# Optimization experiments

Measured on AMD Instinct MI355X. Metric: run time of the kernel, lower is better.

The kernel has to match this reference:

```python
import jax, jax.numpy as jnp
import numpy as np

TAU = 0.01
RHO = 1.99
SIGMA = 1.0 / TAU / 72.0  # 1/tau/72 as in __init__
N_IT = 10  # n_it_max


def nabla2(x):
    # forward finite differences: channel 0 along W (last axis), channel 1 along H
    u = jnp.zeros(x.shape + (2,), x.dtype)
    u = u.at[..., :, :-1, 0].add(x[..., :, 1:] - x[..., :, :-1])
    u = u.at[..., :-1, :, 1].add(x[..., 1:, :] - x[..., :-1, :])
    return u


def nabla2_adjoint(u):
    x = jnp.zeros(u.shape[:-1], u.dtype)
    x = x.at[..., :, :-1].add(-u[..., :, :-1, 0])
    x = x.at[..., :, 1:].add(u[..., :, :-1, 0])
    x = x.at[..., :-1, :].add(-u[..., :-1, :, 1])
    x = x.at[..., 1:, :].add(u[..., :-1, :, 1])
    return x


def epsilon2(I):
    # Jacobian of the vector field I [..., H, W, 2] -> G [..., H, W, 4]
    I0, I1 = I[..., 0], I[..., 1]
    G = jnp.zeros(I0.shape + (4,), I.dtype)
    G = G.at[..., 0].add(I0)                                  # G0 = I0 - shift_H(I0)
    G = G.at[..., 1:, :, 0].add(-I0[..., :-1, :])
    G = G.at[..., :, 1:, 1].add(I0[..., :, 1:] - I0[..., :, :-1])  # G1: W-diff of I0
    G = G.at[..., 2].add(I1)                                  # G2 = I1 - shift_W(I1)
    G = G.at[..., :, 1:, 2].add(-I1[..., :, :-1])
    G = G.at[..., :-1, :, 3].add(I1[..., 1:, :] - I1[..., :-1, :])  # G3: H-diff of I1
    return G


def epsilon2_adjoint(G):
    I = jnp.zeros(G.shape[:-1] + (2,), G.dtype)
    I = I.at[..., 0].add(G[..., 0])
    I = I.at[..., :-1, :, 0].add(-G[..., 1:, :, 0])
    I = I.at[..., :, :-1, 0].add(-G[..., :, 1:, 1])
    I = I.at[..., :, 1:, 0].add(G[..., :, 1:, 1])
    I = I.at[..., 1].add(G[..., 2])
    I = I.at[..., :, :-1, 1].add(-G[..., :, 1:, 2])
    I = I.at[..., :-1, :, 1].add(-G[..., :-1, :, 3])
    I = I.at[..., 1:, :, 1].add(G[..., :-1, :, 3])
    return I


def setup_inputs() -> dict:
    key = jax.random.key(0)
    y = jax.random.normal(key, (4, 512, 512), dtype=jnp.float32)
    return {"y": y, "ths": 1}


def reference(y, ths):
    lam1 = ths * 0.1
    lam2 = ths * 0.15

    def prox_tau_fr(r):
        left = jnp.sqrt(jnp.sum(r * r, axis=-1)) / (TAU * lam1)
        return r - r / jnp.maximum(left, 1.0)[..., None]

    def prox_sigma_g_conj(u):
        return u / jnp.maximum(jnp.sqrt(jnp.sum(u * u, axis=-1)) / lam2, 1.0)[..., None]

    x2 = y
    r2 = jnp.zeros(y.shape + (2,), y.dtype)
    u2 = jnp.zeros(y.shape + (4,), y.dtype)

    def step(carry, _):
        x2, r2, u2 = carry
        tmp = TAU * epsilon2_adjoint(u2)
        x = (x2 - nabla2_adjoint(tmp) + TAU * y) / (1.0 + TAU)  # prox_tau_fx
        r = prox_tau_fr(r2 + tmp)
        u = prox_sigma_g_conj(
            u2 + SIGMA * epsilon2(nabla2(2.0 * x - x2) - (2.0 * r - r2))
        )
        x2 = x2 + RHO * (x - x2)
        r2 = r2 + RHO * (r - r2)
        u2 = u2 + RHO * (u - u2)
        return (x2, r2, u2), None

    (x2, r2, u2), _ = jax.lax.scan(step, (x2, r2, u2), None, length=N_IT)
    return x2
```

## Files before the change

kernel.cpp:

```cpp
#include <hip/hip_runtime.h>
#include <hip/hip_fp16.h>
#include <math.h>

#define HH 512
#define WW 512
#define BB 4
#define NPIX (BB * HH * WW)

#define HS 4
#define NSX 9
#define NBAND (HH / HS)
#define NWAVES (NSX * NBAND * BB)
#define NBLK (NWAVES / 4)
#define BPR (NBLK / 8)

constexpr float TAUf   = 0.01f;
constexpr float RHOf   = 1.99f;
constexpr float SIGMAf = (float)(1.0 / 0.01 / 72.0);
constexpr float INV1PT = (float)(1.0 / 1.01);

__device__ __forceinline__ float SD(float v) { return __shfl_down(v, 1, 64); }
__device__ __forceinline__ unsigned SDu(unsigned v) { return __shfl_down(v, 1, 64); }
__device__ __forceinline__ float SUp(float v) { return __shfl_up(v, 1, 64); }

__device__ __forceinline__ int swiz_wid(int bid, int tid) {
    return (((bid & 7) * BPR) + (bid >> 3)) * 4 + (tid >> 6);
}


template <int MODE>
__global__ __launch_bounds__(256) void sweep(
    const float* __restrict__ y, const int* __restrict__ ths_p,
    const uint2* __restrict__ f_in, const uint2* __restrict__ u_in,
    uint2* __restrict__ f_out, uint2* __restrict__ u_out,
    float* __restrict__ xout)
{
    const int tid  = threadIdx.x;
    const int lane = tid & 63;
    const int wid  = swiz_wid(blockIdx.x, tid);
    const int sx   = wid % NSX;
    const int t2   = wid / NSX;
    const int band = t2 & (NBAND - 1);
    const int b    = t2 / NBAND;
    const int R0   = band * HS;
    const int w    = sx * 60 - 2 + lane;
    const int boff = b * (HH * WW);
    const bool wok = ((unsigned)w) < (unsigned)WW;
    const float mA = (w >= 1 && w < WW) ? 1.f : 0.f;
    const float mB = (w >= 0 && w < WW - 1) ? 1.f : 0.f;
    const bool cok = (lane >= 2) && (lane < 62) && (w < WW);

    const float ths  = (float)ths_p[0];
    const float tl1_ = TAUf * (ths * 0.1f);
    const float l2_  = ths * 0.15f;

    float uf0[4], uf1[4], uf2[4], uf3[4];
    unsigned u12r[4];
    float i0r[2], i1r[2];
    float sr[2], t1r[2];
    float v0r[4], v1r[2];
    #pragma unroll
    for (int q = 0; q < 4; ++q) { uf0[q]=uf1[q]=uf2[q]=uf3[q]=0.f; v0r[q]=0.f; u12r[q]=0u; }
    i0r[0]=i0r[1]=i1r[0]=i1r[1]=0.f;
    sr[0]=sr[1]=0.f; t1r[0]=t1r[1]=0.f; v1r[0]=v1r[1]=0.f;

    auto uload = [&](int row) -> uint2 {
        uint2 z; z.x = 0u; z.y = 0u;
        if (((unsigned)row) < (unsigned)HH && wok)
            z = u_in[(size_t)(boff + row * WW + w)];
        return z;
    };
    auto fload = [&](int row) -> uint2 {
        uint2 z; z.x = 0u; z.y = 0u;
        if (((unsigned)row) < (unsigned)HH && wok)
            z = f_in[(size_t)(boff + row * WW + w)];
        return z;
    };
    auto unpk = [&](int slot, uint2 raw) {
        __half2 lo = *(reinterpret_cast<__half2*>(&raw.x));
        __half2 hi = *(reinterpret_cast<__half2*>(&raw.y));
        uf0[slot] = __low2float(lo); uf1[slot] = __high2float(lo);
        uf2[slot] = __low2float(hi); uf3[slot] = __high2float(hi);
        u12r[slot] = (raw.x >> 16) | (raw.y << 16);
    };
    auto compI = [&](int rr, int islot, int c, int d, int uu_) {
        if (((unsigned)rr) < (unsigned)HH) {
            float hD  = (rr < HH - 1) ? 1.f : 0.f;
            unsigned pp = SDu(u12r[c]);
            __half2 ph = *(reinterpret_cast<__half2*>(&pp));
            float u1n = __low2float(ph);
            float u2n = __high2float(ph);
            i0r[islot] = uf0[c] - uf0[d] - u1n + mA * uf1[c];
            i1r[islot] = uf2[c] - u2n - hD * uf3[c] + uf3[uu_];
        } else { i0r[islot] = 0.f; i1r[islot] = 0.f; }
    };

    if (MODE == 2) {
        unpk(2, uload(R0 - 2));
        unpk(3, uload(R0 - 1));
        unpk(0, uload(R0));
        compI(R0 - 1, 1, 3, 0, 2);
        uint2 puA = uload(R0 + 1);
        uint2 puB = uload(R0 + 2);
        uint2 pfA = fload(R0);
        uint2 pfB = fload(R0 + 1);
        #pragma unroll
        for (int k = 0; k < HS; ++k) {
            const int rr = R0 + k;
            unpk((k + 1) & 3, puA);
            puA = puB;
            if (k < HS - 2) puB = uload(R0 + k + 3);
            __half2 lo = *(reinterpret_cast<__half2*>(&pfA.x));
            __half2 hi = *(reinterpret_cast<__half2*>(&pfA.y));
            float x2v = __low2float(lo);
            float yv  = __high2float(hi);
            pfA = pfB;
            if (k < HS - 2) pfB = fload(R0 + k + 2);
            compI(rr, k & 1, k & 3, (k + 1) & 3, (k + 3) & 3);
            float hD = (rr < HH - 1) ? 1.f : 0.f;
            float i0c = i0r[k & 1], i1c = i1r[k & 1], i1u = i1r[(k + 1) & 1];
            float i0l = SUp(i0c);
            float na = TAUf * (mA * i0l - mB * i0c + i1u - hD * i1c);
            float x = (x2v - na + TAUf * yv) * INV1PT;
            if (cok) xout[boff + rr * WW + w] = x2v + RHOf * (x - x2v);
        }
        return;
    }

    auto compS = [&](int rr, int isc, int isp,
                     float yv, float x2v, float r20v, float r21v, unsigned yraw,
                     bool coreRow, float &sOut, float &t0Out, float &t1Out) {
        if (((unsigned)rr) < (unsigned)HH) {
            float hD = (rr < HH - 1) ? 1.f : 0.f;
            float i0c = i0r[isc], i1c = i1r[isc], i1u = i1r[isp];
            float i0l = SUp(i0c);
            float na = TAUf * (mA * i0l - mB * i0c + i1u - hD * i1c);
            float x = (x2v - na + TAUf * yv) * INV1PT;
            float rr0 = r20v + TAUf * i0c;
            float rr1 = r21v + TAUf * i1c;
            float d = rr0 * rr0 + rr1 * rr1;
            float rinv = fminf(tl1_ * __builtin_amdgcn_rsqf(d), 1.0f);
            float r0 = rr0 - rr0 * rinv;
            float r1 = rr1 - rr1 * rinv;
            sOut  = 2.f * x  - x2v;
            t0Out = 2.f * r0 - r20v;
            t1Out = 2.f * r1 - r21v;
            if (coreRow && cok) {
                int idx = boff + rr * WW + w;
                __half2 lo2 = __floats2half2_rn(x2v + RHOf * (x - x2v),
                                                r20v + RHOf * (r0 - r20v));
                unsigned r1b = (unsigned)__half_as_ushort(
                    __float2half(r21v + RHOf * (r1 - r21v)));
                uint2 st; st.x = *(unsigned*)&lo2; st.y = r1b | (yraw << 16);
                f_out[(size_t)idx] = st;
            }
        } else { sOut = 0.f; t0Out = 0.f; t1Out = 0.f; }
    };

    auto compU = [&](int ro, int v0c_s, int v0u_s, int v1c_s, int v1d_s, int uslot) {
        float hD  = (ro < HH - 1) ? 1.f : 0.f;
        float v0c = v0r[v0c_s], v0u = v0r[v0u_s];
        float v1c = v1r[v1c_s], v1d = v1r[v1d_s];
        float v0l = SUp(v0c);
        float v1l = SUp(v1c);
        float G0 = v0c - v0u;
        float G1 = mA * (v0c - v0l);
        float G2 = v1c - mA * v1l;
        float G3 = hD * (v1d - v1c);
        float u0v = uf0[uslot], u1v = uf1[uslot], u2v = uf2[uslot], u3v = uf3[uslot];
        float uu0 = u0v + SIGMAf * G0;
        float uu1 = u1v + SIGMAf * G1;
        float uu2 = u2v + SIGMAf * G2;
        float uu3 = u3v + SIGMAf * G3;
        float d = uu0 * uu0 + uu1 * uu1 + uu2 * uu2 + uu3 * uu3;
        float ui = fminf(l2_ * __builtin_amdgcn_rsqf(d), 1.0f);
        if (cok) {
            int idx = boff + ro * WW + w;
            __half2 lo = __floats2half2_rn(u0v + RHOf * (uu0 * ui - u0v),
                                           u1v + RHOf * (uu1 * ui - u1v));
            __half2 hi = __floats2half2_rn(u2v + RHOf * (uu2 * ui - u2v),
                                           u3v + RHOf * (uu3 * ui - u3v));
            uint2 st; st.x = *(unsigned*)&lo; st.y = *(unsigned*)&hi;
            u_out[(size_t)idx] = st;
        }
    };

    uint2 puA, puB, pfA, pfB;
    puA.x = puA.y = puB.x = puB.y = 0u;
    pfA.x = pfA.y = pfB.x = pfB.y = 0u;
    unpk(1, uload(R0 - 3));
    unpk(2, uload(R0 - 2));
    unpk(3, uload(R0 - 1));
    compI(R0 - 2, 0, 2, 3, 1);
    puA = uload(R0);
    puB = uload(R0 + 1);
    pfA = fload(R0 - 1);
    pfB = fload(R0);

    #pragma unroll
    for (int k = 0; k < HS + 3; ++k) {
        const int rr = R0 - 1 + k;
        unpk(k & 3, puA);
        puA = puB;
        if (k <= HS) puB = uload(R0 + k + 2);
        __half2 lo = *(reinterpret_cast<__half2*>(&pfA.x));
        __half2 hi = *(reinterpret_cast<__half2*>(&pfA.y));
        float x2v  = __low2float(lo);
        float r20v = __high2float(lo);
        float r21v = __low2float(hi);
        float yv   = __high2float(hi);
        unsigned yraw = pfA.y >> 16;
        pfA = pfB;
        if (k <= HS) pfB = fload(R0 + k + 1);

        compI(rr, (k + 1) & 1, (k + 3) & 3, k & 3, (k + 2) & 3);

        float sN, t0N, t1N;
        compS(rr, (k + 1) & 1, k & 1, yv, x2v, r20v, r21v, yraw,
              (k >= 1 && k <= HS), sN, t0N, t1N);

        {
            float sPrev  = sr[k & 1];
            float t1Prev = t1r[k & 1];
            float hDm1   = (rr < HH) ? 1.f : 0.f;
            v0r[(k + 3) & 3] = mB * (SD(sN) - sN) - t0N;
            v1r[k & 1]       = hDm1 * (sN - sPrev) - t1Prev;
            sr[(k + 1) & 1]  = sN;
            t1r[(k + 1) & 1] = t1N;
        }

        if (k >= 3) compU(R0 - 3 + k, (k + 1) & 3, k & 3, (k + 1) & 1, k & 1,
                          (k + 1) & 3);
    }
}

__global__ __launch_bounds__(256) void fused01(
    const float* __restrict__ y, const int* __restrict__ ths_p,
    uint2* __restrict__ f_out, uint2* __restrict__ u_out)
{
    const int tid  = threadIdx.x;
    const int lane = tid & 63;
    const int wid  = swiz_wid(blockIdx.x, tid);
    const int sx   = wid % NSX;
    const int t2   = wid / NSX;
    const int band = t2 & (NBAND - 1);
    const int b    = t2 / NBAND;
    const int R0   = band * HS;
    const int w    = sx * 58 - 3 + lane;
    const int boff = b * (HH * WW);
    const bool wok = ((unsigned)w) < (unsigned)WW;
    const float mA = (w >= 1 && w < WW) ? 1.f : 0.f;
    const float mB = (w >= 0 && w < WW - 1) ? 1.f : 0.f;
    const bool cok = (lane >= 3) && (lane <= 60) && (w < WW);

    const float ths  = (float)ths_p[0];
    const float tl1_ = TAUf * (ths * 0.1f);
    const float l2_  = ths * 0.15f;

    float p0r[4];
    float p1r[2];
    float yD1 = 0.f, yD2 = 0.f, yD3 = 0.f;

    float uf0[4], uf1[4], uf2[4], uf3[4];
    unsigned u12r[4];
    float i0r[2], i1r[2];
    float sr[2], t1r[2];
    float v0r[4], v1r[2];
    #pragma unroll
    for (int q = 0; q < 4; ++q) {
        uf0[q]=uf1[q]=uf2[q]=uf3[q]=0.f; v0r[q]=0.f; u12r[q]=0u; p0r[q]=0.f;
    }
    i0r[0]=i0r[1]=i1r[0]=i1r[1]=0.f;
    sr[0]=sr[1]=0.f; t1r[0]=t1r[1]=0.f; v1r[0]=v1r[1]=0.f; p1r[0]=p1r[1]=0.f;

    auto yload = [&](int row) -> float {
        return (((unsigned)row) < (unsigned)HH && wok)
                   ? y[boff + row * WW + w] : 0.f;
    };
    auto unpk = [&](int slot, uint2 raw) {
        __half2 lo = *(reinterpret_cast<__half2*>(&raw.x));
        __half2 hi = *(reinterpret_cast<__half2*>(&raw.y));
        uf0[slot] = __low2float(lo); uf1[slot] = __high2float(lo);
        uf2[slot] = __low2float(hi); uf3[slot] = __high2float(hi);
        u12r[slot] = (raw.x >> 16) | (raw.y << 16);
    };
    auto compI = [&](int rr, int islot, int c, int d, int uu_) {
        if (((unsigned)rr) < (unsigned)HH) {
            float hD  = (rr < HH - 1) ? 1.f : 0.f;
            unsigned pp = SDu(u12r[c]);
            __half2 ph = *(reinterpret_cast<__half2*>(&pp));
            float u1n = __low2float(ph);
            float u2n = __high2float(ph);
            i0r[islot] = uf0[c] - uf0[d] - u1n + mA * uf1[c];
            i1r[islot] = uf2[c] - u2n - hD * uf3[c] + uf3[uu_];
        } else { i0r[islot] = 0.f; i1r[islot] = 0.f; }
    };

    float pyA = yload(R0 - 4);
    float pyB = yload(R0 - 3);

    #pragma unroll
    for (int j = 0; j < HS + 9; ++j) {
        const int p = R0 - 4 + j;
        float yp = pyA; pyA = pyB;
        if (j <= HS + 6) pyB = yload(R0 - 2 + j);

        p0r[j & 3]       = mB * (SD(yp) - yp);
        p1r[(j + 1) & 1] = ((p < HH) ? 1.f : 0.f) * (yp - yD1);

        if (j >= 3) {
            const int ro = R0 - 6 + j;
            float hD  = (ro < HH - 1) ? 1.f : 0.f;
            float v0c = p0r[(j + 2) & 3], v0u = p0r[(j + 1) & 3];
            float v1c = p1r[j & 1],       v1d = p1r[(j + 1) & 1];
            float G0 = v0c - v0u;
            float G1 = mA * (v0c - SUp(v0c));
            float G2 = v1c - mA * SUp(v1c);
            float G3 = hD * (v1d - v1c);
            float uu0 = SIGMAf * G0, uu1 = SIGMAf * G1;
            float uu2 = SIGMAf * G2, uu3 = SIGMAf * G3;
            float d = uu0*uu0 + uu1*uu1 + uu2*uu2 + uu3*uu3;
            float ui = fminf(l2_ * __builtin_amdgcn_rsqf(d), 1.0f);
            __half2 lo = __floats2half2_rn(RHOf * (uu0 * ui), RHOf * (uu1 * ui));
            __half2 hi = __floats2half2_rn(RHOf * (uu2 * ui), RHOf * (uu3 * ui));
            uint2 st; st.x = *(unsigned*)&lo; st.y = *(unsigned*)&hi;
            unpk((j + 2) & 3, st);
        }

        if (j == 5) compI(R0 - 2, 0, 2, 3, 1);

        if (j >= 6) {
            const int k  = j - 6;
            const int rr = R0 - 1 + k;
            __half yh = __float2half(yD3);
            float yv  = __half2float(yh);
            unsigned yraw = (unsigned)__half_as_ushort(yh);

            compI(rr, (k + 1) & 1, (k + 3) & 3, k & 3, (k + 2) & 3);

            float sN, t0N, t1N;
            {
                const bool coreRow = (k >= 1 && k <= HS);
                if (((unsigned)rr) < (unsigned)HH) {
                    float hD = (rr < HH - 1) ? 1.f : 0.f;
                    float i0c = i0r[(k + 1) & 1], i1c = i1r[(k + 1) & 1];
                    float i1u = i1r[k & 1];
                    float i0l = SUp(i0c);
                    float na = TAUf * (mA * i0l - mB * i0c + i1u - hD * i1c);
                    float x = (yv - na + TAUf * yv) * INV1PT;
                    float rr0 = TAUf * i0c;
                    float rr1 = TAUf * i1c;
                    float d2 = rr0*rr0 + rr1*rr1;
                    float rinv = fminf(tl1_ * __builtin_amdgcn_rsqf(d2), 1.0f);
                    float r0 = rr0 - rr0 * rinv;
                    float r1 = rr1 - rr1 * rinv;
                    sN  = 2.f * x - yv;
                    t0N = 2.f * r0;
                    t1N = 2.f * r1;
                    if (coreRow && cok) {
                        int idx = boff + rr * WW + w;
                        __half2 lo2 = __floats2half2_rn(yv + RHOf * (x - yv),
                                                        RHOf * r0);
                        unsigned r1b = (unsigned)__half_as_ushort(
                            __float2half(RHOf * r1));
                        uint2 st2; st2.x = *(unsigned*)&lo2;
                        st2.y = r1b | (yraw << 16);
                        f_out[(size_t)idx] = st2;
                    }
                } else { sN = 0.f; t0N = 0.f; t1N = 0.f; }
            }

            {
                float sPrev  = sr[k & 1];
                float t1Prev = t1r[k & 1];
                float hDm1   = (rr < HH) ? 1.f : 0.f;
                v0r[(k + 3) & 3] = mB * (SD(sN) - sN) - t0N;
                v1r[k & 1]       = hDm1 * (sN - sPrev) - t1Prev;
                sr[(k + 1) & 1]  = sN;
                t1r[(k + 1) & 1] = t1N;
            }

            if (k >= 3) {
                const int ro = R0 - 3 + k;
                float hD  = (ro < HH - 1) ? 1.f : 0.f;
                float v0c = v0r[(k + 1) & 3], v0u = v0r[k & 3];
                float v1c = v1r[(k + 1) & 1], v1d = v1r[k & 1];
                float v0l = SUp(v0c);
                float v1l = SUp(v1c);
                float G0 = v0c - v0u;
                float G1 = mA * (v0c - v0l);
                float G2 = v1c - mA * v1l;
                float G3 = hD * (v1d - v1c);
                const int us = (k + 1) & 3;
                float u0v = uf0[us], u1v = uf1[us], u2v = uf2[us], u3v = uf3[us];
                float uu0 = u0v + SIGMAf * G0;
                float uu1 = u1v + SIGMAf * G1;
                float uu2 = u2v + SIGMAf * G2;
                float uu3 = u3v + SIGMAf * G3;
                float d = uu0*uu0 + uu1*uu1 + uu2*uu2 + uu3*uu3;
                float ui = fminf(l2_ * __builtin_amdgcn_rsqf(d), 1.0f);
                if (cok) {
                    int idx = boff + ro * WW + w;
                    __half2 lo = __floats2half2_rn(u0v + RHOf * (uu0 * ui - u0v),
                                                   u1v + RHOf * (uu1 * ui - u1v));
                    __half2 hi = __floats2half2_rn(u2v + RHOf * (uu2 * ui - u2v),
                                                   u3v + RHOf * (uu3 * ui - u3v));
                    uint2 st; st.x = *(unsigned*)&lo; st.y = *(unsigned*)&hi;
                    u_out[(size_t)idx] = st;
                }
            }
        }

        yD3 = yD2; yD2 = yD1; yD1 = yp;
    }
}

__global__ __launch_bounds__(256) void fused89(
    const int* __restrict__ ths_p,
    const uint2* __restrict__ f_in, const uint2* __restrict__ u_in,
    float* __restrict__ xout)
{
    const int tid  = threadIdx.x;
    const int lane = tid & 63;
    const int wid  = swiz_wid(blockIdx.x, tid);
    const int sx   = wid % NSX;
    const int t2   = wid / NSX;
    const int band = t2 & (NBAND - 1);
    const int b    = t2 / NBAND;
    const int R0   = band * HS;
    const int R0p  = R0 - 2;
    const int w    = sx * 58 - 3 + lane;
    const int boff = b * (HH * WW);
    const bool wok = ((unsigned)w) < (unsigned)WW;
    const float mA = (w >= 1 && w < WW) ? 1.f : 0.f;
    const float mB = (w >= 0 && w < WW - 1) ? 1.f : 0.f;
    const bool cokC = (lane >= 3) && (lane <= 60) && (w < WW);

    const float ths  = (float)ths_p[0];
    const float tl1_ = TAUf * (ths * 0.1f);
    const float l2_  = ths * 0.15f;

    constexpr int HSp = HS + 3;

    float uf0[4], uf1[4], uf2[4], uf3[4];
    unsigned u12r[4];
    float i0r[2], i1r[2];
    float sr[2], t1r[2];
    float v0r[4], v1r[2];
    float cf0[4], cf1[4], cf2[4], cf3[4];
    unsigned c12[4];
    float ci0[2], ci1[2];
    uint2 fmid[4];
    #pragma unroll
    for (int q = 0; q < 4; ++q) {
        uf0[q]=uf1[q]=uf2[q]=uf3[q]=0.f; v0r[q]=0.f; u12r[q]=0u;
        cf0[q]=cf1[q]=cf2[q]=cf3[q]=0.f; c12[q]=0u;
        fmid[q].x = 0u; fmid[q].y = 0u;
    }
    i0r[0]=i0r[1]=i1r[0]=i1r[1]=0.f;
    ci0[0]=ci0[1]=ci1[0]=ci1[1]=0.f;
    sr[0]=sr[1]=0.f; t1r[0]=t1r[1]=0.f; v1r[0]=v1r[1]=0.f;

    auto uload = [&](int row) -> uint2 {
        uint2 z; z.x = 0u; z.y = 0u;
        if (((unsigned)row) < (unsigned)HH && wok)
            z = u_in[(size_t)(boff + row * WW + w)];
        return z;
    };
    auto fload = [&](int row) -> uint2 {
        uint2 z; z.x = 0u; z.y = 0u;
        if (((unsigned)row) < (unsigned)HH && wok)
            z = f_in[(size_t)(boff + row * WW + w)];
        return z;
    };
    auto unpk = [&](int slot, uint2 raw) {
        __half2 lo = *(reinterpret_cast<__half2*>(&raw.x));
        __half2 hi = *(reinterpret_cast<__half2*>(&raw.y));
        uf0[slot] = __low2float(lo); uf1[slot] = __high2float(lo);
        uf2[slot] = __low2float(hi); uf3[slot] = __high2float(hi);
        u12r[slot] = (raw.x >> 16) | (raw.y << 16);
    };
    auto compI = [&](int rr, int islot, int c, int d, int uu_) {
        if (((unsigned)rr) < (unsigned)HH) {
            float hD  = (rr < HH - 1) ? 1.f : 0.f;
            unsigned pp = SDu(u12r[c]);
            __half2 ph = *(reinterpret_cast<__half2*>(&pp));
            float u1n = __low2float(ph);
            float u2n = __high2float(ph);
            i0r[islot] = uf0[c] - uf0[d] - u1n + mA * uf1[c];
            i1r[islot] = uf2[c] - u2n - hD * uf3[c] + uf3[uu_];
        } else { i0r[islot] = 0.f; i1r[islot] = 0.f; }
    };
    auto cunpk = [&](int slot, uint2 raw) {
        __half2 lo = *(reinterpret_cast<__half2*>(&raw.x));
        __half2 hi = *(reinterpret_cast<__half2*>(&raw.y));
        cf0[slot] = __low2float(lo); cf1[slot] = __high2float(lo);
        cf2[slot] = __low2float(hi); cf3[slot] = __high2float(hi);
        c12[slot] = (raw.x >> 16) | (raw.y << 16);
    };
    auto ccompI = [&](int rr, int islot, int c, int d, int uu_) {
        if (((unsigned)rr) < (unsigned)HH) {
            float hD  = (rr < HH - 1) ? 1.f : 0.f;
            unsigned pp = SDu(c12[c]);
            __half2 ph = *(reinterpret_cast<__half2*>(&pp));
            float u1n = __low2float(ph);
            float u2n = __high2float(ph);
            ci0[islot] = cf0[c] - cf0[d] - u1n + mA * cf1[c];
            ci1[islot] = cf2[c] - u2n - hD * cf3[c] + cf3[uu_];
        } else { ci0[islot] = 0.f; ci1[islot] = 0.f; }
    };

    unpk(1, uload(R0p - 3));
    unpk(2, uload(R0p - 2));
    unpk(3, uload(R0p - 1));
    compI(R0p - 2, 0, 2, 3, 1);
    uint2 puA = uload(R0p);
    uint2 puB = uload(R0p + 1);
    uint2 pfA = fload(R0p - 1);
    uint2 pfB = fload(R0p);

    #pragma unroll
    for (int J = 0; J < HSp + 3; ++J) {
        const int rp = R0p - 1 + J;

        unpk(J & 3, puA);
        puA = puB;
        if (J <= HSp) puB = uload(R0p + J + 2);
        __half2 flo = *(reinterpret_cast<__half2*>(&pfA.x));
        __half2 fhi = *(reinterpret_cast<__half2*>(&pfA.y));
        float x2v  = __low2float(flo);
        float r20v = __high2float(flo);
        float r21v = __low2float(fhi);
        float yv   = __high2float(fhi);
        unsigned yraw = pfA.y >> 16;
        pfA = pfB;
        if (J <= HSp) pfB = fload(R0p + J + 1);

        compI(rp, (J + 1) & 1, (J + 3) & 3, J & 3, (J + 2) & 3);

        float sN, t0N, t1N;
        if (((unsigned)rp) < (unsigned)HH) {
            float hD = (rp < HH - 1) ? 1.f : 0.f;
            float i0c = i0r[(J + 1) & 1], i1c = i1r[(J + 1) & 1];
            float i1u = i1r[J & 1];
            float i0l = SUp(i0c);
            float na = TAUf * (mA * i0l - mB * i0c + i1u - hD * i1c);
            float x = (x2v - na + TAUf * yv) * INV1PT;
            float rr0 = r20v + TAUf * i0c;
            float rr1 = r21v + TAUf * i1c;
            float d = rr0 * rr0 + rr1 * rr1;
            float rinv = fminf(tl1_ * __builtin_amdgcn_rsqf(d), 1.0f);
            float r0 = rr0 - rr0 * rinv;
            float r1 = rr1 - rr1 * rinv;
            sN  = 2.f * x  - x2v;
            t0N = 2.f * r0 - r20v;
            t1N = 2.f * r1 - r21v;
            if (J >= 3 && J <= HS + 2) {
                __half2 lo2 = __floats2half2_rn(x2v + RHOf * (x - x2v),
                                                r20v + RHOf * (r0 - r20v));
                unsigned r1b = (unsigned)__half_as_ushort(
                    __float2half(r21v + RHOf * (r1 - r21v)));
                uint2 st; st.x = *(unsigned*)&lo2; st.y = r1b | (yraw << 16);
                fmid[(J + 1) & 3] = st;
            }
        } else { sN = 0.f; t0N = 0.f; t1N = 0.f; }

        {
            float sPrev  = sr[J & 1];
            float t1Prev = t1r[J & 1];
            float hDm1   = (rp < HH) ? 1.f : 0.f;
            v0r[(J + 3) & 3] = mB * (SD(sN) - sN) - t0N;
            v1r[J & 1]       = hDm1 * (sN - sPrev) - t1Prev;
            sr[(J + 1) & 1]  = sN;
            t1r[(J + 1) & 1] = t1N;
        }

        if (J >= 3) {
            const int ro = R0p - 3 + J;
            float hD  = (ro < HH - 1) ? 1.f : 0.f;
            float v0c = v0r[(J + 1) & 3], v0u = v0r[J & 3];
            float v1c = v1r[(J + 1) & 1], v1d = v1r[J & 1];
            float v0l = SUp(v0c);
            float v1l = SUp(v1c);
            float G0 = v0c - v0u;
            float G1 = mA * (v0c - v0l);
            float G2 = v1c - mA * v1l;
            float G3 = hD * (v1d - v1c);
            const int us = (J + 1) & 3;
            float u0v = uf0[us], u1v = uf1[us], u2v = uf2[us], u3v = uf3[us];
            float uu0 = u0v + SIGMAf * G0;
            float uu1 = u1v + SIGMAf * G1;
            float uu2 = u2v + SIGMAf * G2;
            float uu3 = u3v + SIGMAf * G3;
            float d = uu0*uu0 + uu1*uu1 + uu2*uu2 + uu3*uu3;
            float ui = fminf(l2_ * __builtin_amdgcn_rsqf(d), 1.0f);
            uint2 st; st.x = 0u; st.y = 0u;
            if (((unsigned)ro) < (unsigned)HH) {
                __half2 lo = __floats2half2_rn(u0v + RHOf * (uu0 * ui - u0v),
                                               u1v + RHOf * (uu1 * ui - u1v));
                __half2 hi = __floats2half2_rn(u2v + RHOf * (uu2 * ui - u2v),
                                               u3v + RHOf * (uu3 * ui - u3v));
                st.x = *(unsigned*)&lo; st.y = *(unsigned*)&hi;
            }
            cunpk((J + 3) & 3, st);
        }

        if (J == 5) ccompI(R0 - 1, 1, 3, 0, 2);
        if (J >= 6) {
            const int kc = J - 6;
            const int rc = R0 + kc;
            ccompI(rc, kc & 1, kc & 3, (kc + 1) & 3, (kc + 3) & 3);
            uint2 fm = fmid[(J + 2) & 3];
            __half2 mlo = *(reinterpret_cast<__half2*>(&fm.x));
            __half2 mhi = *(reinterpret_cast<__half2*>(&fm.y));
            float cx2 = __low2float(mlo);
            float cyv = __high2float(mhi);
            float hD = (rc < HH - 1) ? 1.f : 0.f;
            float i0c = ci0[kc & 1], i1c = ci1[kc & 1], i1u = ci1[(kc + 1) & 1];
            float i0l = SUp(i0c);
            float na = TAUf * (mA * i0l - mB * i0c + i1u - hD * i1c);
            float x = (cx2 - na + TAUf * cyv) * INV1PT;
            if (cokC) xout[boff + rc * WW + w] = cx2 + RHOf * (x - cx2);
        }
    }
}

extern "C" void kernel_launch(void* const* d_in, const int* in_sizes, int n_in,
                              void* d_out, int out_size, void* d_ws, size_t ws_size,
                              hipStream_t stream)
{
    const float* y   = (const float*)d_in[0];
    const int*   ths = (const int*)d_in[1];
    uint2* ws2 = (uint2*)d_ws;

    uint2* FA = ws2;
    uint2* UA = ws2 + (size_t)NPIX;
    uint2* FB = ws2 + 2 * (size_t)NPIX;
    uint2* UB = ws2 + 3 * (size_t)NPIX;
    float* xout = (float*)d_out;

    dim3 block(256);
    dim3 grid(NBLK);

    fused01<<<grid, block, 0, stream>>>(y, ths, FA, UA);
    uint2 *fi = FA, *ui = UA, *fo = FB, *uo = UB;
    for (int it = 2; it <= 7; ++it) {
        sweep<1><<<grid, block, 0, stream>>>(y, ths, fi, ui, fo, uo, nullptr);
        uint2* t;
        t = fi; fi = fo; fo = t;
        t = ui; ui = uo; uo = t;
    }
    fused89<<<grid, block, 0, stream>>>(ths, fi, ui, xout);
}
```

Measured before the change: 137.3 us.

## Process two adjacent pixels per lane in middle sweep with 16-byte accesses

```diff
diff --git a/kernel.cpp b/kernel.cpp
--- a/kernel.cpp
+++ b/kernel.cpp
@@ -14,6 +14,11 @@
 #define NBLK (NWAVES / 4)
 #define BPR (NBLK / 8)
 
+#define NSX2 5
+#define NWAVES2 (NSX2 * NBAND * BB)
+#define NBLK2 (NWAVES2 / 2)
+#define BPR2 (NBLK2 / 8)
+
 constexpr float TAUf   = 0.01f;
 constexpr float RHOf   = 1.99f;
 constexpr float SIGMAf = (float)(1.0 / 0.01 / 72.0);
@@ -23,214 +28,229 @@
 __device__ __forceinline__ unsigned SDu(unsigned v) { return __shfl_down(v, 1, 64); }
 __device__ __forceinline__ float SUp(float v) { return __shfl_up(v, 1, 64); }
 
-__device__ __forceinline__ int swiz_wid(int bid, int tid) {
-    return (((bid & 7) * BPR) + (bid >> 3)) * 4 + (tid >> 6);
-}
-
-
-template <int MODE>
-__global__ __launch_bounds__(256) void sweep(
-    const float* __restrict__ y, const int* __restrict__ ths_p,
+
+__global__ __launch_bounds__(128) void sweep2(
+    const int* __restrict__ ths_p,
     const uint2* __restrict__ f_in, const uint2* __restrict__ u_in,
-    uint2* __restrict__ f_out, uint2* __restrict__ u_out,
-    float* __restrict__ xout)
+    uint2* __restrict__ f_out, uint2* __restrict__ u_out)
 {
     const int tid  = threadIdx.x;
     const int lane = tid & 63;
-    const int wid  = swiz_wid(blockIdx.x, tid);
-    const int sx   = wid % NSX;
-    const int t2   = wid / NSX;
+    const int bid  = blockIdx.x;
+    const int wid  = (((bid & 7) * BPR2) + (bid >> 3)) * 2 + (tid >> 6);
+    const int sx   = wid % NSX2;
+    const int t2   = wid / NSX2;
     const int band = t2 & (NBAND - 1);
     const int b    = t2 / NBAND;
     const int R0   = band * HS;
-    const int w    = sx * 60 - 2 + lane;
+    const int wA   = sx * 124 - 2 + 2 * lane;
+    const int wB   = wA + 1;
     const int boff = b * (HH * WW);
-    const bool wok = ((unsigned)w) < (unsigned)WW;
-    const float mA = (w >= 1 && w < WW) ? 1.f : 0.f;
-    const float mB = (w >= 0 && w < WW - 1) ? 1.f : 0.f;
-    const bool cok = (lane >= 2) && (lane < 62) && (w < WW);
+    const bool okA = ((unsigned)wA) < (unsigned)WW;
+    const float mAA = (wA >= 1 && wA < WW) ? 1.f : 0.f;
+    const float mAB = (wB >= 1 && wB < WW) ? 1.f : 0.f;
+    const float mBA = (wA >= 0 && wA < WW - 1) ? 1.f : 0.f;
+    const float mBB = (wB >= 0 && wB < WW - 1) ? 1.f : 0.f;
+    const bool cok = (lane >= 1) && (lane <= 62) && okA;
 
     const float ths  = (float)ths_p[0];
     const float tl1_ = TAUf * (ths * 0.1f);
     const float l2_  = ths * 0.15f;
 
-    float uf0[4], uf1[4], uf2[4], uf3[4];
-    unsigned u12r[4];
-    float i0r[2], i1r[2];
-    float sr[2], t1r[2];
-    float v0r[4], v1r[2];
+    float uf0A[4], uf1A[4], uf2A[4], uf3A[4];
+    float uf0B[4], uf1B[4], uf2B[4], uf3B[4];
+    unsigned u12A[4];
+    float i0A[2], i1A[2], i0B[2], i1B[2];
+    float sA[2], sB[2], t1A[2], t1B[2];
+    float v0A[4], v0B[4], v1A[2], v1B[2];
     #pragma unroll
-    for (int q = 0; q < 4; ++q) { uf0[q]=uf1[q]=uf2[q]=uf3[q]=0.f; v0r[q]=0.f; u12r[q]=0u; }
-    i0r[0]=i0r[1]=i1r[0]=i1r[1]=0.f;
-    sr[0]=sr[1]=0.f; t1r[0]=t1r[1]=0.f; v1r[0]=v1r[1]=0.f;
-
-    auto uload = [&](int row) -> uint2 {
-        uint2 z; z.x = 0u; z.y = 0u;
-        if (((unsigned)row) < (unsigned)HH && wok)
-            z = u_in[(size_t)(boff + row * WW + w)];
+    for (int q = 0; q < 4; ++q) {
+        uf0A[q]=uf1A[q]=uf2A[q]=uf3A[q]=0.f;
+        uf0B[q]=uf1B[q]=uf2B[q]=uf3B[q]=0.f;
+        v0A[q]=v0B[q]=0.f; u12A[q]=0u;
+    }
+    i0A[0]=i0A[1]=i1A[0]=i1A[1]=0.f;
+    i0B[0]=i0B[1]=i1B[0]=i1B[1]=0.f;
+    sA[0]=sA[1]=sB[0]=sB[1]=0.f;
+    t1A[0]=t1A[1]=t1B[0]=t1B[1]=0.f;
+    v1A[0]=v1A[1]=v1B[0]=v1B[1]=0.f;
+
+    auto uload2 = [&](int row) -> uint4 {
+        uint4 z; z.x=z.y=z.z=z.w=0u;
+        if (((unsigned)row) < (unsigned)HH && okA)
+            z = *(const uint4*)(u_in + (size_t)(boff + row * WW + wA));
         return z;
     };
-    auto fload = [&](int row) -> uint2 {
-        uint2 z; z.x = 0u; z.y = 0u;
-        if (((unsigned)row) < (unsigned)HH && wok)
-            z = f_in[(size_t)(boff + row * WW + w)];
+    auto fload2 = [&](int row) -> uint4 {
+        uint4 z; z.x=z.y=z.z=z.w=0u;
+        if (((unsigned)row) < (unsigned)HH && okA)
+            z = *(const uint4*)(f_in + (size_t)(boff + row * WW + wA));
         return z;
     };
-    auto unpk = [&](int slot, uint2 raw) {
-        __half2 lo = *(reinterpret_cast<__half2*>(&raw.x));
-        __half2 hi = *(reinterpret_cast<__half2*>(&raw.y));
-        uf0[slot] = __low2float(lo); uf1[slot] = __high2float(lo);
-        uf2[slot] = __low2float(hi); uf3[slot] = __high2float(hi);
-        u12r[slot] = (raw.x >> 16) | (raw.y << 16);
-    };
-    auto compI = [&](int rr, int islot, int c, int d, int uu_) {
+    auto unpk2 = [&](int slot, uint4 raw) {
+        __half2 a0 = *(reinterpret_cast<__half2*>(&raw.x));
+        __half2 a1 = *(reinterpret_cast<__half2*>(&raw.y));
+        __half2 b0 = *(reinterpret_cast<__half2*>(&raw.z));
+        __half2 b1 = *(reinterpret_cast<__half2*>(&raw.w));
+        uf0A[slot] = __low2float(a0); uf1A[slot] = __high2float(a0);
+        uf2A[slot] = __low2float(a1); uf3A[slot] = __high2float(a1);
+        uf0B[slot] = __low2float(b0); uf1B[slot] = __high2float(b0);
+        uf2B[slot] = __low2float(b1); uf3B[slot] = __high2float(b1);
+        u12A[slot] = (raw.x >> 16) | (raw.y << 16);
+    };
+    auto compI2 = [&](int rr, int islot, int c, int d, int uu_) {
         if (((unsigned)rr) < (unsigned)HH) {
             float hD  = (rr < HH - 1) ? 1.f : 0.f;
-            unsigned pp = SDu(u12r[c]);
+            unsigned pp = SDu(u12A[c]);
             __half2 ph = *(reinterpret_cast<__half2*>(&pp));
-            float u1n = __low2float(ph);
-            float u2n = __high2float(ph);
-            i0r[islot] = uf0[c] - uf0[d] - u1n + mA * uf1[c];
-            i1r[islot] = uf2[c] - u2n - hD * uf3[c] + uf3[uu_];
-        } else { i0r[islot] = 0.f; i1r[islot] = 0.f; }
-    };
-
-    if (MODE == 2) {
-        unpk(2, uload(R0 - 2));
-        unpk(3, uload(R0 - 1));
-        unpk(0, uload(R0));
-        compI(R0 - 1, 1, 3, 0, 2);
-        uint2 puA = uload(R0 + 1);
-        uint2 puB = uload(R0 + 2);
-        uint2 pfA = fload(R0);
-        uint2 pfB = fload(R0 + 1);
-        #pragma unroll
-        for (int k = 0; k < HS; ++k) {
-            const int rr = R0 + k;
-            unpk((k + 1) & 3, puA);
-            puA = puB;
-            if (k < HS - 2) puB = uload(R0 + k + 3);
-            __half2 lo = *(reinterpret_cast<__half2*>(&pfA.x));
-            __half2 hi = *(reinterpret_cast<__half2*>(&pfA.y));
-            float x2v = __low2float(lo);
-            float yv  = __high2float(hi);
-            pfA = pfB;
-            if (k < HS - 2) pfB = fload(R0 + k + 2);
-            compI(rr, k & 1, k & 3, (k + 1) & 3, (k + 3) & 3);
-            float hD = (rr < HH - 1) ? 1.f : 0.f;
-            float i0c = i0r[k & 1], i1c = i1r[k & 1], i1u = i1r[(k + 1) & 1];
-            float i0l = SUp(i0c);
-            float na = TAUf * (mA * i0l - mB * i0c + i1u - hD * i1c);
-            float x = (x2v - na + TAUf * yv) * INV1PT;
-            if (cok) xout[boff + rr * WW + w] = x2v + RHOf * (x - x2v);
-        }
-        return;
-    }
-
-    auto compS = [&](int rr, int isc, int isp,
-                     float yv, float x2v, float r20v, float r21v, unsigned yraw,
-                     bool coreRow, float &sOut, float &t0Out, float &t1Out) {
-        if (((unsigned)rr) < (unsigned)HH) {
-            float hD = (rr < HH - 1) ? 1.f : 0.f;
-            float i0c = i0r[isc], i1c = i1r[isc], i1u = i1r[isp];
-            float i0l = SUp(i0c);
-            float na = TAUf * (mA * i0l - mB * i0c + i1u - hD * i1c);
-            float x = (x2v - na + TAUf * yv) * INV1PT;
-            float rr0 = r20v + TAUf * i0c;
-            float rr1 = r21v + TAUf * i1c;
-            float d = rr0 * rr0 + rr1 * rr1;
-            float rinv = fminf(tl1_ * __builtin_amdgcn_rsqf(d), 1.0f);
-            float r0 = rr0 - rr0 * rinv;
-            float r1 = rr1 - rr1 * rinv;
-            sOut  = 2.f * x  - x2v;
-            t0Out = 2.f * r0 - r20v;
-            t1Out = 2.f * r1 - r21v;
-            if (coreRow && cok) {
-                int idx = boff + rr * WW + w;
-                __half2 lo2 = __floats2half2_rn(x2v + RHOf * (x - x2v),
-                                                r20v + RHOf * (r0 - r20v));
-                unsigned r1b = (unsigned)__half_as_ushort(
-                    __float2half(r21v + RHOf * (r1 - r21v)));
-                uint2 st; st.x = *(unsigned*)&lo2; st.y = r1b | (yraw << 16);
-                f_out[(size_t)idx] = st;
-            }
-        } else { sOut = 0.f; t0Out = 0.f; t1Out = 0.f; }
-    };
-
-    auto compU = [&](int ro, int v0c_s, int v0u_s, int v1c_s, int v1d_s, int uslot) {
-        float hD  = (ro < HH - 1) ? 1.f : 0.f;
-        float v0c = v0r[v0c_s], v0u = v0r[v0u_s];
-        float v1c = v1r[v1c_s], v1d = v1r[v1d_s];
-        float v0l = SUp(v0c);
-        float v1l = SUp(v1c);
-        float G0 = v0c - v0u;
-        float G1 = mA * (v0c - v0l);
-        float G2 = v1c - mA * v1l;
-        float G3 = hD * (v1d - v1c);
-        float u0v = uf0[uslot], u1v = uf1[uslot], u2v = uf2[uslot], u3v = uf3[uslot];
-        float uu0 = u0v + SIGMAf * G0;
-        float uu1 = u1v + SIGMAf * G1;
-        float uu2 = u2v + SIGMAf * G2;
-        float uu3 = u3v + SIGMAf * G3;
-        float d = uu0 * uu0 + uu1 * uu1 + uu2 * uu2 + uu3 * uu3;
-        float ui = fminf(l2_ * __builtin_amdgcn_rsqf(d), 1.0f);
-        if (cok) {
-            int idx = boff + ro * WW + w;
-            __half2 lo = __floats2half2_rn(u0v + RHOf * (uu0 * ui - u0v),
-                                           u1v + RHOf * (uu1 * ui - u1v));
-            __half2 hi = __floats2half2_rn(u2v + RHOf * (uu2 * ui - u2v),
-                                           u3v + RHOf * (uu3 * ui - u3v));
-            uint2 st; st.x = *(unsigned*)&lo; st.y = *(unsigned*)&hi;
-            u_out[(size_t)idx] = st;
-        }
-    };
-
-    uint2 puA, puB, pfA, pfB;
-    puA.x = puA.y = puB.x = puB.y = 0u;
-    pfA.x = pfA.y = pfB.x = pfB.y = 0u;
-    unpk(1, uload(R0 - 3));
-    unpk(2, uload(R0 - 2));
-    unpk(3, uload(R0 - 1));
-    compI(R0 - 2, 0, 2, 3, 1);
-    puA = uload(R0);
-    puB = uload(R0 + 1);
-    pfA = fload(R0 - 1);
-    pfB = fload(R0);
+            float u1nB = __low2float(ph);
+            float u2nB = __high2float(ph);
+            i0A[islot] = uf0A[c] - uf0A[d] - uf1B[c] + mAA * uf1A[c];
+            i1A[islot] = uf2A[c] - uf2B[c] - hD * uf3A[c] + uf3A[uu_];
+            i0B[islot] = uf0B[c] - uf0B[d] - u1nB + mAB * uf1B[c];
+            i1B[islot] = uf2B[c] - u2nB - hD * uf3B[c] + uf3B[uu_];
+        } else {
+            i0A[islot]=0.f; i1A[islot]=0.f; i0B[islot]=0.f; i1B[islot]=0.f;
+        }
+    };
+
+    unpk2(1, uload2(R0 - 3));
+    unpk2(2, uload2(R0 - 2));
+    unpk2(3, uload2(R0 - 1));
+    compI2(R0 - 2, 0, 2, 3, 1);
+    uint4 puA = uload2(R0);
+    uint4 puB = uload2(R0 + 1);
+    uint4 pfA = fload2(R0 - 1);
+    uint4 pfB = fload2(R0);
 
     #pragma unroll
     for (int k = 0; k < HS + 3; ++k) {
         const int rr = R0 - 1 + k;
-        unpk(k & 3, puA);
+
+        unpk2(k & 3, puA);
         puA = puB;
-        if (k <= HS) puB = uload(R0 + k + 2);
-        __half2 lo = *(reinterpret_cast<__half2*>(&pfA.x));
-        __half2 hi = *(reinterpret_cast<__half2*>(&pfA.y));
-        float x2v  = __low2float(lo);
-        float r20v = __high2float(lo);
-        float r21v = __low2float(hi);
-        float yv   = __high2float(hi);
-        unsigned yraw = pfA.y >> 16;
+        if (k <= HS) puB = uload2(R0 + k + 2);
+
+        __half2 fa0 = *(reinterpret_cast<__half2*>(&pfA.x));
+        __half2 fa1 = *(reinterpret_cast<__half2*>(&pfA.y));
+        __half2 fb0 = *(reinterpret_cast<__half2*>(&pfA.z));
+        __half2 fb1 = *(reinterpret_cast<__half2*>(&pfA.w));
+        float x2A = __low2float(fa0), r0A_ = __high2float(fa0);
+        float r1A_ = __low2float(fa1), yA = __high2float(fa1);
+        float x2B = __low2float(fb0), r0B_ = __high2float(fb0);
+        float r1B_ = __low2float(fb1), yB = __high2float(fb1);
+        unsigned yrawA = pfA.y >> 16;
+        unsigned yrawB = pfA.w >> 16;
         pfA = pfB;
-        if (k <= HS) pfB = fload(R0 + k + 1);
-
-        compI(rr, (k + 1) & 1, (k + 3) & 3, k & 3, (k + 2) & 3);
-
-        float sN, t0N, t1N;
-        compS(rr, (k + 1) & 1, k & 1, yv, x2v, r20v, r21v, yraw,
-              (k >= 1 && k <= HS), sN, t0N, t1N);
-
+        if (k <= HS) pfB = fload2(R0 + k + 1);
+
+        compI2(rr, (k + 1) & 1, (k + 3) & 3, k & 3, (k + 2) & 3);
+
+        float sNA, t0NA, t1NA, sNB, t0NB, t1NB;
+        uint2 FAo, FBo; FAo.x=FAo.y=FBo.x=FBo.y=0u;
         {
-            float sPrev  = sr[k & 1];
-            float t1Prev = t1r[k & 1];
-            float hDm1   = (rr < HH) ? 1.f : 0.f;
-            v0r[(k + 3) & 3] = mB * (SD(sN) - sN) - t0N;
-            v1r[k & 1]       = hDm1 * (sN - sPrev) - t1Prev;
-            sr[(k + 1) & 1]  = sN;
-            t1r[(k + 1) & 1] = t1N;
-        }
-
-        if (k >= 3) compU(R0 - 3 + k, (k + 1) & 3, k & 3, (k + 1) & 1, k & 1,
-                          (k + 1) & 3);
+            const int isc = (k + 1) & 1, isp = k & 1;
+            if (((unsigned)rr) < (unsigned)HH) {
+                float hD = (rr < HH - 1) ? 1.f : 0.f;
+                float i0cA = i0A[isc], i1cA = i1A[isc], i1uA = i1A[isp];
+                float i0cB = i0B[isc], i1cB = i1B[isc], i1uB = i1B[isp];
+                float i0lA = SUp(i0B[isc]);
+                float i0lB = i0A[isc];
+                float naA = TAUf * (mAA * i0lA - mBA * i0cA + i1uA - hD * i1cA);
+                float naB = TAUf * (mAB * i0lB - mBB * i0cB + i1uB - hD * i1cB);
+                float xA = (x2A - naA + TAUf * yA) * INV1PT;
+                float xB = (x2B - naB + TAUf * yB) * INV1PT;
+                float rrA0 = r0A_ + TAUf * i0cA, rrA1 = r1A_ + TAUf * i1cA;
+                float rrB0 = r0B_ + TAUf * i0cB, rrB1 = r1B_ + TAUf * i1cB;
+                float dA = rrA0*rrA0 + rrA1*rrA1;
+                float dB = rrB0*rrB0 + rrB1*rrB1;
+                float riA = fminf(tl1_ * __builtin_amdgcn_rsqf(dA), 1.0f);
+                float riB = fminf(tl1_ * __builtin_amdgcn_rsqf(dB), 1.0f);
+                float r0nA = rrA0 - rrA0 * riA, r1nA = rrA1 - rrA1 * riA;
+                float r0nB = rrB0 - rrB0 * riB, r1nB = rrB1 - rrB1 * riB;
+                sNA  = 2.f * xA - x2A; t0NA = 2.f * r0nA - r0A_; t1NA = 2.f * r1nA - r1A_;
+                sNB  = 2.f * xB - x2B; t0NB = 2.f * r0nB - r0B_; t1NB = 2.f * r1nB - r1B_;
+                __half2 la = __floats2half2_rn(x2A + RHOf * (xA - x2A),
+                                               r0A_ + RHOf * (r0nA - r0A_));
+                unsigned r1bA = (unsigned)__half_as_ushort(
+                    __float2half(r1A_ + RHOf * (r1nA - r1A_)));
+                __half2 lb = __floats2half2_rn(x2B + RHOf * (xB - x2B),
+                                               r0B_ + RHOf * (r0nB - r0B_));
+                unsigned r1bB = (unsigned)__half_as_ushort(
+                    __float2half(r1B_ + RHOf * (r1nB - r1B_)));
+                FAo.x = *(unsigned*)&la; FAo.y = r1bA | (yrawA << 16);
+                FBo.x = *(unsigned*)&lb; FBo.y = r1bB | (yrawB << 16);
+                if ((k >= 1 && k <= HS) && cok) {
+                    int idx = boff + rr * WW + wA;
+                    uint4 st; st.x = FAo.x; st.y = FAo.y; st.z = FBo.x; st.w = FBo.y;
+                    *(uint4*)(f_out + (size_t)idx) = st;
+                }
+            } else {
+                sNA=0.f; t0NA=0.f; t1NA=0.f; sNB=0.f; t0NB=0.f; t1NB=0.f;
+            }
+        }
+
+        {
+            float sPA = sA[k & 1], t1PA = t1A[k & 1];
+            float sPB = sB[k & 1], t1PB = t1B[k & 1];
+            float hDm1 = (rr < HH) ? 1.f : 0.f;
+            float sdA = SD(sNA);
+            v0A[(k + 3) & 3] = mBA * (sNB - sNA) - t0NA;
+            v0B[(k + 3) & 3] = mBB * (sdA - sNB) - t0NB;
+            v1A[k & 1] = hDm1 * (sNA - sPA) - t1PA;
+            v1B[k & 1] = hDm1 * (sNB - sPB) - t1PB;
+            sA[(k + 1) & 1] = sNA; sB[(k + 1) & 1] = sNB;
+            t1A[(k + 1) & 1] = t1NA; t1B[(k + 1) & 1] = t1NB;
+        }
+
+        if (k >= 3) {
+            const int ro = R0 - 3 + k;
+            const int v0c_s = (k + 1) & 3, v0u_s = k & 3;
+            const int v1c_s = (k + 1) & 1, v1d_s = k & 1;
+            const int us = (k + 1) & 3;
+            float hD  = (ro < HH - 1) ? 1.f : 0.f;
+            float v0cA = v0A[v0c_s], v0uA = v0A[v0u_s];
+            float v1cA = v1A[v1c_s], v1dA = v1A[v1d_s];
+            float v0cB = v0B[v0c_s], v0uB = v0B[v0u_s];
+            float v1cB = v1B[v1c_s], v1dB = v1B[v1d_s];
+            float v0lA = SUp(v0B[v0c_s]);
+            float v1lA = SUp(v1B[v1c_s]);
+            float v0lB = v0cA;
+            float v1lB = v1cA;
+            float G0A = v0cA - v0uA;
+            float G1A = mAA * (v0cA - v0lA);
+            float G2A = v1cA - mAA * v1lA;
+            float G3A = hD * (v1dA - v1cA);
+            float G0B = v0cB - v0uB;
+            float G1B = mAB * (v0cB - v0lB);
+            float G2B = v1cB - mAB * v1lB;
+            float G3B = hD * (v1dB - v1cB);
+            float u0A_ = uf0A[us], u1A_ = uf1A[us], u2A_ = uf2A[us], u3A_ = uf3A[us];
+            float u0B_ = uf0B[us], u1B_ = uf1B[us], u2B_ = uf2B[us], u3B_ = uf3B[us];
+            float a0 = u0A_ + SIGMAf * G0A, a1 = u1A_ + SIGMAf * G1A;
+            float a2 = u2A_ + SIGMAf * G2A, a3 = u3A_ + SIGMAf * G3A;
+            float b0 = u0B_ + SIGMAf * G0B, b1 = u1B_ + SIGMAf * G1B;
+            float b2 = u2B_ + SIGMAf * G2B, b3 = u3B_ + SIGMAf * G3B;
+            float dA = a0*a0 + a1*a1 + a2*a2 + a3*a3;
+            float dB = b0*b0 + b1*b1 + b2*b2 + b3*b3;
+            float uiA = fminf(l2_ * __builtin_amdgcn_rsqf(dA), 1.0f);
+            float uiB = fminf(l2_ * __builtin_amdgcn_rsqf(dB), 1.0f);
+            if (cok) {
+                int idx = boff + ro * WW + wA;
+                __half2 la = __floats2half2_rn(u0A_ + RHOf * (a0 * uiA - u0A_),
+                                               u1A_ + RHOf * (a1 * uiA - u1A_));
+                __half2 ha = __floats2half2_rn(u2A_ + RHOf * (a2 * uiA - u2A_),
+                                               u3A_ + RHOf * (a3 * uiA - u3A_));
+                __half2 lb = __floats2half2_rn(u0B_ + RHOf * (b0 * uiB - u0B_),
+                                               u1B_ + RHOf * (b1 * uiB - u1B_));
+                __half2 hb = __floats2half2_rn(u2B_ + RHOf * (b2 * uiB - u2B_),
+                                               u3B_ + RHOf * (b3 * uiB - u3B_));
+                uint4 st;
+                st.x = *(unsigned*)&la; st.y = *(unsigned*)&ha;
+                st.z = *(unsigned*)&lb; st.w = *(unsigned*)&hb;
+                *(uint4*)(u_out + (size_t)idx) = st;
+            }
+        }
     }
 }
 
@@ -240,7 +260,8 @@
 {
     const int tid  = threadIdx.x;
     const int lane = tid & 63;
-    const int wid  = swiz_wid(blockIdx.x, tid);
+    const int bid  = blockIdx.x;
+    const int wid  = (((bid & 7) * BPR) + (bid >> 3)) * 4 + (tid >> 6);
     const int sx   = wid % NSX;
     const int t2   = wid / NSX;
     const int band = t2 & (NBAND - 1);
@@ -422,7 +443,8 @@
 {
     const int tid  = threadIdx.x;
     const int lane = tid & 63;
-    const int wid  = swiz_wid(blockIdx.x, tid);
+    const int bid  = blockIdx.x;
+    const int wid  = (((bid & 7) * BPR) + (bid >> 3)) * 4 + (tid >> 6);
     const int sx   = wid % NSX;
     const int t2   = wid / NSX;
     const int band = t2 & (NBAND - 1);
@@ -639,16 +661,13 @@
     uint2* UB = ws2 + 3 * (size_t)NPIX;
     float* xout = (float*)d_out;
 
-    dim3 block(256);
-    dim3 grid(NBLK);
-
-    fused01<<<grid, block, 0, stream>>>(y, ths, FA, UA);
+    fused01<<<dim3(NBLK), dim3(256), 0, stream>>>(y, ths, FA, UA);
     uint2 *fi = FA, *ui = UA, *fo = FB, *uo = UB;
     for (int it = 2; it <= 7; ++it) {
-        sweep<1><<<grid, block, 0, stream>>>(y, ths, fi, ui, fo, uo, nullptr);
+        sweep2<<<dim3(NBLK2), dim3(128), 0, stream>>>(ths, fi, ui, fo, uo);
         uint2* t;
         t = fi; fi = fo; fo = t;
         t = ui; ui = uo; uo = t;
     }
-    fused89<<<grid, block, 0, stream>>>(ths, fi, ui, xout);
+    fused89<<<dim3(NBLK), dim3(256), 0, stream>>>(ths, fi, ui, xout);
 }
```

Result: slower. 142.6 us (+3.8%).
